# Performance work log

Measured on AMD Instinct MI355X. Metric: run time of the kernel, lower is better.

## Reference

```python
import jax, jax.numpy as jnp
import numpy as np

GRID_SIZE = 0.08
EPS = 1e-5
B, N, C_IN, C_OUT = 8, 65536, 64, 128


def setup_inputs() -> dict:
    key = jax.random.key(0)
    k1, k2, k3, k4 = jax.random.split(key, 4)
    # xyz in [0, 2): ~25 voxels per axis at grid_size=0.08 -> M ~ 15k clusters
    xyz = jax.random.uniform(k1, (B, N, 3), dtype=jnp.float32) * 2.0
    feats = jax.random.normal(k2, (B, N, C_IN), dtype=jnp.float32)
    W = jax.random.normal(k3, (C_IN, C_OUT), dtype=jnp.float32) / np.sqrt(C_IN)
    b = jnp.zeros((C_OUT,), jnp.float32)
    gamma = jnp.ones((C_OUT,), jnp.float32)
    beta = jnp.zeros((C_OUT,), jnp.float32)
    return {"xyz": xyz, "feats": feats, "W": W, "b": b, "gamma": gamma, "beta": beta}


def _voxel_pool_one(xyz_b, feats_b):
    # xyz_b: (N,3), feats_b: (N,C). Static pad to N clusters (worst case M=N).
    n = xyz_b.shape[0]
    coords = jnp.floor(xyz_b / GRID_SIZE).astype(jnp.int32)
    coords = coords - coords.min(axis=0)
    dims = coords.max(axis=0) + 1
    keys = coords[:, 0] * dims[1] * dims[2] + coords[:, 1] * dims[2] + coords[:, 2]
    # unique(return_inverse) via sort: cluster ids follow ascending key order
    order = jnp.argsort(keys)
    sk = keys[order]
    is_new = jnp.concatenate([jnp.ones((1,), bool), sk[1:] != sk[:-1]])
    seg = (jnp.cumsum(is_new) - 1).astype(jnp.int32)
    cluster = jnp.zeros((n,), jnp.int32).at[order].set(seg)
    M = is_new.sum().astype(jnp.int32)
    xyz_sum = jax.ops.segment_sum(xyz_b, cluster, num_segments=n)
    feat_sum = jax.ops.segment_sum(feats_b, cluster, num_segments=n)
    count = jax.ops.segment_sum(jnp.ones((n,), xyz_b.dtype), cluster, num_segments=n)
    count = jnp.maximum(count, 1.0)[:, None]
    return xyz_sum / count, feat_sum / count, cluster, M


def reference(xyz, feats, W, b, gamma, beta):
    xyz_pooled, feat_mean, cluster, Ms = jax.vmap(_voxel_pool_one)(xyz, feats)
    max_M = Ms.max()
    # linear + layernorm on (B, N, C_OUT) (padded rows beyond M_b are zeros)
    h = feat_mean @ W + b
    mu = h.mean(axis=-1, keepdims=True)
    var = ((h - mu) ** 2).mean(axis=-1, keepdims=True)
    feats_pooled = (h - mu) * jax.lax.rsqrt(var + EPS) * gamma + beta
    return xyz_pooled, feats_pooled, cluster, max_M
```

## Files before the change

### kernel.cpp

```cpp
#include <hip/hip_runtime.h>
#include <cstdint>
#include <climits>
#include <math.h>

#define Bb    8
#define Nn    65536
#define CIN   64
#define COUT  128
#define KMAXX 15632
#define VKEY  25600
#define VSTR  25600
#define EPSV  1e-5f

#define OFF_MVALS  0
#define OFF_MAXM   8
#define OFF_TAB    16
#define OFF_CNT    204816
#define OFF_SEGS   329872
#define OFF_SORT   454928
#define OFF_MEAN   586000
#define WS_END     8589584
#define MEMSET_INTS 204816

__device__ __forceinline__ int voxc(float x, float rcp_g) {
    return (int)floorf(x * rcp_g);
}

__device__ __forceinline__ float rdlanef(float v, int l) {
    return __uint_as_float(__builtin_amdgcn_readlane(__float_as_uint(v), l));
}

__global__ __launch_bounds__(256) void k_zero(float4* __restrict__ feats4,
                                              float4* __restrict__ xyz4) {
    const unsigned A_PER_B = 49904u * 32u;
    const unsigned B_PER_B = 49904u * 3u / 4u;
    const unsigned A4 = Bb * A_PER_B;
    const unsigned TOT = A4 + Bb * B_PER_B;
    unsigned t = blockIdx.x * 256u + threadIdx.x;
    if (t >= TOT) return;
    const float4 z = make_float4(0.f, 0.f, 0.f, 0.f);
    if (t < A4) {
        unsigned b = t / A_PER_B;
        unsigned r = t - b * A_PER_B;
        feats4[(size_t)b * (Nn * 32u) + 15632u * 32u + r] = z;
    } else {
        unsigned t2 = t - A4;
        unsigned b = t2 / B_PER_B;
        unsigned r = t2 - b * B_PER_B;
        xyz4[(size_t)b * (Nn * 3u / 4u) + (15632u * 3u / 4u) + r] = z;
    }
}

__global__ __launch_bounds__(256) void k_count(const float* __restrict__ xyz,
                                               int* __restrict__ tab,
                                               float grid) {
    float rcp_g = __builtin_amdgcn_rcpf(grid);
    int i = blockIdx.x * 256 + threadIdx.x;
    int b = i >> 16;
    int c0 = voxc(xyz[(size_t)i * 3 + 0], rcp_g);
    int c1 = voxc(xyz[(size_t)i * 3 + 1], rcp_g);
    int c2 = voxc(xyz[(size_t)i * 3 + 2], rcp_g);
    atomicAdd(&tab[b * VSTR + (c0 * 32 + c1) * 32 + c2], 1);
}

__global__ __launch_bounds__(1024) void k_scan(int* __restrict__ tab,
                                               float* __restrict__ cntf,
                                               int* __restrict__ segs,
                                               int* __restrict__ Ms,
                                               int* __restrict__ maxM) {
    __shared__ int wsC[16], wsFg[16];
    int b = blockIdx.x, tid = threadIdx.x;
    int lane = tid & 63, wv = tid >> 6;
    bool act = tid < (VKEY / 32);
    int4 f[8];
    int4* tb4 = (int4*)(tab + b * VSTR);
    const int4 z4 = make_int4(0, 0, 0, 0);
#pragma unroll
    for (int j = 0; j < 8; ++j) f[j] = act ? tb4[tid * 8 + j] : z4;
    int* ff = (int*)f;
    int sc = 0, sf = 0;
#pragma unroll
    for (int j = 0; j < 32; ++j) { sc += ff[j]; sf += (ff[j] != 0); }
    int ic = sc, ig = sf;
#pragma unroll
    for (int d = 1; d < 64; d <<= 1) {
        int tc = __shfl_up(ic, d);
        int tg = __shfl_up(ig, d);
        if (lane >= d) { ic += tc; ig += tg; }
    }
    if (lane == 63) { wsC[wv] = ic; wsFg[wv] = ig; }
    __syncthreads();
    int wpC = 0, wpF = 0, totF = 0;
#pragma unroll
    for (int w = 0; w < 16; ++w) {
        int vc = wsC[w], vf = wsFg[w];
        if (w < wv) { wpC += vc; wpF += vf; }
        totF += vf;
    }
    if (act) {
        int runC = wpC + ic - sc;
        int runF = wpF + ig - sf;
        int4 o[8];
        int* oo = (int*)o;
#pragma unroll
        for (int j = 0; j < 32; ++j) {
            int c = ff[j];
            oo[j] = (runF << 17) | runC;
            if (c) {
                cntf[b * KMAXX + runF] = (float)c;
                segs[b * KMAXX + runF] = runC;
                runC += c;
                runF += 1;
            }
        }
#pragma unroll
        for (int j = 0; j < 8; ++j) tb4[tid * 8 + j] = o[j];
    }
    if (tid == 0) {
        Ms[b] = totF;
        atomicMax(maxM, totF);
    }
}

__global__ __launch_bounds__(256) void k_scatter(const float* __restrict__ xyz,
                                                 int* __restrict__ tab,
                                                 unsigned short* __restrict__ sorted,
                                                 float* __restrict__ out_cluster,
                                                 float grid) {
    float rcp_g = __builtin_amdgcn_rcpf(grid);
    int i = blockIdx.x * 256 + threadIdx.x;
    int b = i >> 16;
    int c0 = voxc(xyz[(size_t)i * 3 + 0], rcp_g);
    int c1 = voxc(xyz[(size_t)i * 3 + 1], rcp_g);
    int c2 = voxc(xyz[(size_t)i * 3 + 2], rcp_g);
    int v = atomicAdd(&tab[b * VSTR + (c0 * 32 + c1) * 32 + c2], 1);
    sorted[(size_t)b * Nn + (v & 0x1FFFF)] = (unsigned short)i;
    out_cluster[i] = (float)(v >> 17);
}

#define GPB 245
__global__ __launch_bounds__(256, 6) void k_gather(const float* __restrict__ xyz,
                                                   const float4* __restrict__ feats4,
                                                   const unsigned short* __restrict__ sorted,
                                                   const float* __restrict__ cnt,
                                                   const int* __restrict__ segs,
                                                   const int* __restrict__ Ms,
                                                   float4* __restrict__ mean4,
                                                   float* __restrict__ out_xyz) {
    const int b = blockIdx.x / GPB;
    const int blk = blockIdx.x - b * GPB;
    const int wv = threadIdx.x >> 6, lane = threadIdx.x & 63;
    const int sub = lane >> 4, c4 = lane & 15;
    const int rowBase = blk * 64 + wv * 16;
    if (rowBase >= KMAXX) return;
    const int M = Ms[b];
    const size_t pbase = (size_t)b * Nn;
    const size_t cbase = (size_t)b * KMAXX;
    float cl = 0.0f;
    int sl = 0;
    if (lane < 16) {
        int r = rowBase + lane;
        if (r < M) { cl = cnt[cbase + r]; sl = segs[cbase + r]; }
    }
    for (int it = 0; it < 4; ++it) {
        const int row0 = rowBase + it * 4;
        int c[4], s[4];
        float cf[4];
#pragma unroll
        for (int q = 0; q < 4; ++q) {
            cf[q] = rdlanef(cl, it * 4 + q);
            s[q] = __builtin_amdgcn_readlane(sl, it * 4 + q);
            c[q] = (int)cf[q];
        }
        int p[4][2];
#pragma unroll
        for (int q = 0; q < 4; ++q) {
            p[q][0] = (sub     < c[q]) ? (int)sorted[pbase + s[q] + sub]     : -1;
            p[q][1] = (sub + 4 < c[q]) ? (int)sorted[pbase + s[q] + sub + 4] : -1;
        }
        float4 acc[4];
        float axs[4];
#pragma unroll
        for (int q = 0; q < 4; ++q) { acc[q] = make_float4(0.f, 0.f, 0.f, 0.f); axs[q] = 0.f; }
#pragma unroll
        for (int q = 0; q < 4; ++q) {
#pragma unroll
            for (int h = 0; h < 2; ++h) {
                int pp = p[q][h];
                if (pp >= 0) {
                    float4 v = feats4[(pbase + pp) * 16 + c4];
                    acc[q].x += v.x; acc[q].y += v.y; acc[q].z += v.z; acc[q].w += v.w;
                    if (c4 < 3) axs[q] += xyz[(pbase + pp) * 3 + c4];
                }
            }
        }
#pragma unroll
        for (int q = 0; q < 4; ++q) {
            for (int g = 2; g * 4 < c[q]; ++g) {
                int i = g * 4 + sub;
                if (i < c[q]) {
                    int pp = (int)sorted[pbase + s[q] + i];
                    float4 v = feats4[(pbase + pp) * 16 + c4];
                    acc[q].x += v.x; acc[q].y += v.y; acc[q].z += v.z; acc[q].w += v.w;
                    if (c4 < 3) axs[q] += xyz[(pbase + pp) * 3 + c4];
                }
            }
        }
#pragma unroll
        for (int q = 0; q < 4; ++q) {
            const int row = row0 + q;
            if (row < M) {
                float4 a = acc[q];
                a.x += __shfl_xor(a.x, 16); a.x += __shfl_xor(a.x, 32);
                a.y += __shfl_xor(a.y, 16); a.y += __shfl_xor(a.y, 32);
                a.z += __shfl_xor(a.z, 16); a.z += __shfl_xor(a.z, 32);
                a.w += __shfl_xor(a.w, 16); a.w += __shfl_xor(a.w, 32);
                float ax = axs[q];
                ax += __shfl_xor(ax, 16); ax += __shfl_xor(ax, 32);
                float cv = cf[q];
                float4 m4 = make_float4(a.x / cv, a.y / cv, a.z / cv, a.w / cv);
                if (lane < 16) mean4[(cbase + row) * 16 + c4] = m4;
                if (lane < 3)
                    out_xyz[(pbase + row) * 3 + lane] = ax / cv;
            } else {
                if (lane < 3)
                    out_xyz[(pbase + row) * 3 + lane] = 0.0f;
            }
        }
    }
}

#define BPB 245
__global__ __launch_bounds__(256) void k_gemmln(const float4* __restrict__ mean4,
                                                const int* __restrict__ Ms,
                                                const int* __restrict__ maxM,
                                                const float* __restrict__ W,
                                                const float* __restrict__ bias,
                                                const float* __restrict__ gamma,
                                                const float* __restrict__ beta,
                                                float* __restrict__ out_feats,
                                                float* __restrict__ out_maxM) {
    __shared__ float sWT[128 * 68];
    const int tid = threadIdx.x;
    for (int idx = tid; idx < 64 * 128; idx += 256) {
        int k = idx >> 7, c = idx & 127;
        sWT[c * 68 + k] = W[idx];
    }
    if (blockIdx.x == 0 && tid == 0) out_maxM[0] = (float)maxM[0];
    const int b = blockIdx.x / BPB;
    const int blk = blockIdx.x - b * BPB;
    const int wv = tid >> 6, lane = tid & 63;
    const int c4 = lane & 15;
    const int M = Ms[b];
    const float bias0 = bias[lane], bias1 = bias[lane + 64];
    const float g0 = gamma[lane], g1 = gamma[lane + 64];
    const float be0 = beta[lane], be1 = beta[lane + 64];
    __syncthreads();
    const int rowBase = blk * 64 + wv * 16;
    if (rowBase >= KMAXX) return;
    const size_t cbase = (size_t)b * KMAXX;
    if (rowBase >= M) {
        const float4 z = make_float4(0.f, 0.f, 0.f, 0.f);
        float4* of4 = (float4*)out_feats;
        size_t obase = ((size_t)b * Nn + rowBase) * 32;
#pragma unroll
        for (int i = 0; i < 8; ++i) of4[obase + i * 64 + lane] = z;
        return;
    }
    const float* wt0 = &sWT[lane * 68];
    const float* wt1 = &sWT[(lane + 64) * 68];
    for (int it = 0; it < 4; ++it) {
        const int row0 = rowBase + it * 4;
        const size_t cb0 = cbase + row0;
        float4 mm[4];
        bool lv[4];
#pragma unroll
        for (int r = 0; r < 4; ++r) {
            lv[r] = (row0 + r) < M;
            mm[r] = lv[r] ? mean4[(cb0 + r) * 16 + c4]
                          : make_float4(0.f, 0.f, 0.f, 0.f);
        }
        float a0[4] = {bias0, bias0, bias0, bias0};
        float a1[4] = {bias1, bias1, bias1, bias1};
#pragma unroll
        for (int k4 = 0; k4 < 16; ++k4) {
            float4 w0 = *(const float4*)&wt0[k4 * 4];
            float4 w1 = *(const float4*)&wt1[k4 * 4];
#pragma unroll
            for (int r = 0; r < 4; ++r) {
                float s0 = rdlanef(mm[r].x, k4);
                float s1 = rdlanef(mm[r].y, k4);
                float s2 = rdlanef(mm[r].z, k4);
                float s3 = rdlanef(mm[r].w, k4);
                a0[r] += s0 * w0.x + s1 * w0.y + s2 * w0.z + s3 * w0.w;
                a1[r] += s0 * w1.x + s1 * w1.y + s2 * w1.z + s3 * w1.w;
            }
        }
#pragma unroll
        for (int r = 0; r < 4; ++r) {
            float s = a0[r] + a1[r];
#pragma unroll
            for (int d2 = 32; d2 >= 1; d2 >>= 1) s += __shfl_xor(s, d2);
            float mu = s * (1.0f / 128.0f);
            float d0 = a0[r] - mu, d1 = a1[r] - mu;
            float q = d0 * d0 + d1 * d1;
#pragma unroll
            for (int d2 = 32; d2 >= 1; d2 >>= 1) q += __shfl_xor(q, d2);
            float rs = rsqrtf(q * (1.0f / 128.0f) + EPSV);
            float o0 = lv[r] ? (d0 * rs * g0 + be0) : 0.0f;
            float o1 = lv[r] ? (d1 * rs * g1 + be1) : 0.0f;
            size_t ob = ((size_t)b * Nn + row0 + r) * 128;
            out_feats[ob + lane] = o0;
            out_feats[ob + 64 + lane] = o1;
        }
    }
}

extern "C" void kernel_launch(void* const* d_in, const int* in_sizes, int n_in,
                              void* d_out, int out_size, void* d_ws, size_t ws_size,
                              hipStream_t stream) {
    const float* xyz   = (const float*)d_in[0];
    const float* feats = (const float*)d_in[1];
    const float* W     = (const float*)d_in[2];
    const float* bias  = (const float*)d_in[3];
    const float* gamma = (const float*)d_in[4];
    const float* beta  = (const float*)d_in[5];

    float* out = (float*)d_out;
    float* out_xyz     = out;
    float* out_feats   = out + (size_t)Bb * Nn * 3;
    float* out_cluster = out_feats + (size_t)Bb * Nn * COUT;
    float* out_maxM    = out_cluster + (size_t)Bb * Nn;

    int*   wsI    = (int*)d_ws;
    float* wsF    = (float*)d_ws;
    int*   Ms     = wsI + OFF_MVALS;
    int*   maxM   = wsI + OFF_MAXM;
    int*   tab    = wsI + OFF_TAB;
    float* cnt    = wsF + OFF_CNT;
    int*   segs   = wsI + OFF_SEGS;
    unsigned short* sorted = (unsigned short*)(wsI + OFF_SORT);
    float* meanb  = wsF + OFF_MEAN;

    const float grid_sz = 0.08f;

    {
        unsigned tot = Bb * (49904u * 32u) + Bb * (49904u * 3u / 4u);
        k_zero<<<(tot + 255) / 256, 256, 0, stream>>>((float4*)out_feats, (float4*)out_xyz);
    }
    hipMemsetAsync(wsI, 0, (size_t)MEMSET_INTS * 4, stream);
    k_count<<<Bb * Nn / 256, 256, 0, stream>>>(xyz, tab, grid_sz);
    k_scan<<<Bb, 1024, 0, stream>>>(tab, cnt, segs, Ms, maxM);
    k_scatter<<<Bb * Nn / 256, 256, 0, stream>>>(xyz, tab, sorted, out_cluster, grid_sz);
    k_gather<<<Bb * GPB, 256, 0, stream>>>(xyz, (const float4*)feats, sorted, cnt, segs,
                                           Ms, (float4*)meanb, out_xyz);
    k_gemmln<<<Bb * BPB, 256, 0, stream>>>((const float4*)meanb, Ms, maxM, W, bias,
                                           gamma, beta, out_feats, out_maxM);
}
```

Before: 531.4 us.

## Fold padding zero-fill into GEMM-LN kernel and cache voxel keys between passes

Removes the separate zero-fill kernel. The tail rows of out_feats and out_xyz past KMAXX are now zeroed by extra blocks of the GEMM+LayerNorm kernel, whose grid grows to cover all N rows per batch. k_count also stores each point's 16-bit voxel key in workspace, so k_scatter reads the key instead of reloading xyz and recomputing floors. The key buffer aliases the mean buffer, which is safe only because k_gather writes means after k_scatter has consumed the keys.

```diff
diff --git a/kernel.cpp b/kernel.cpp
--- a/kernel.cpp
+++ b/kernel.cpp
@@ -30,29 +30,9 @@
     return __uint_as_float(__builtin_amdgcn_readlane(__float_as_uint(v), l));
 }
 
-__global__ __launch_bounds__(256) void k_zero(float4* __restrict__ feats4,
-                                              float4* __restrict__ xyz4) {
-    const unsigned A_PER_B = 49904u * 32u;
-    const unsigned B_PER_B = 49904u * 3u / 4u;
-    const unsigned A4 = Bb * A_PER_B;
-    const unsigned TOT = A4 + Bb * B_PER_B;
-    unsigned t = blockIdx.x * 256u + threadIdx.x;
-    if (t >= TOT) return;
-    const float4 z = make_float4(0.f, 0.f, 0.f, 0.f);
-    if (t < A4) {
-        unsigned b = t / A_PER_B;
-        unsigned r = t - b * A_PER_B;
-        feats4[(size_t)b * (Nn * 32u) + 15632u * 32u + r] = z;
-    } else {
-        unsigned t2 = t - A4;
-        unsigned b = t2 / B_PER_B;
-        unsigned r = t2 - b * B_PER_B;
-        xyz4[(size_t)b * (Nn * 3u / 4u) + (15632u * 3u / 4u) + r] = z;
-    }
-}
-
 __global__ __launch_bounds__(256) void k_count(const float* __restrict__ xyz,
                                                int* __restrict__ tab,
+                                               unsigned short* __restrict__ keys,
                                                float grid) {
     float rcp_g = __builtin_amdgcn_rcpf(grid);
     int i = blockIdx.x * 256 + threadIdx.x;
@@ -60,7 +40,9 @@
     int c0 = voxc(xyz[(size_t)i * 3 + 0], rcp_g);
     int c1 = voxc(xyz[(size_t)i * 3 + 1], rcp_g);
     int c2 = voxc(xyz[(size_t)i * 3 + 2], rcp_g);
-    atomicAdd(&tab[b * VSTR + (c0 * 32 + c1) * 32 + c2], 1);
+    int key = (c0 * 32 + c1) * 32 + c2;
+    atomicAdd(&tab[b * VSTR + key], 1);
+    keys[i] = (unsigned short)key;
 }
 
 __global__ __launch_bounds__(1024) void k_scan(int* __restrict__ tab,
@@ -122,18 +104,14 @@
     }
 }
 
-__global__ __launch_bounds__(256) void k_scatter(const float* __restrict__ xyz,
+__global__ __launch_bounds__(256) void k_scatter(const unsigned short* __restrict__ keys,
                                                  int* __restrict__ tab,
                                                  unsigned short* __restrict__ sorted,
-                                                 float* __restrict__ out_cluster,
-                                                 float grid) {
-    float rcp_g = __builtin_amdgcn_rcpf(grid);
+                                                 float* __restrict__ out_cluster) {
     int i = blockIdx.x * 256 + threadIdx.x;
     int b = i >> 16;
-    int c0 = voxc(xyz[(size_t)i * 3 + 0], rcp_g);
-    int c1 = voxc(xyz[(size_t)i * 3 + 1], rcp_g);
-    int c2 = voxc(xyz[(size_t)i * 3 + 2], rcp_g);
-    int v = atomicAdd(&tab[b * VSTR + (c0 * 32 + c1) * 32 + c2], 1);
+    int key = keys[i];
+    int v = atomicAdd(&tab[b * VSTR + key], 1);
     sorted[(size_t)b * Nn + (v & 0x1FFFF)] = (unsigned short)i;
     out_cluster[i] = (float)(v >> 17);
 }
@@ -230,7 +208,7 @@
     }
 }
 
-#define BPB 245
+#define GBLK 1024
 __global__ __launch_bounds__(256) void k_gemmln(const float4* __restrict__ mean4,
                                                 const int* __restrict__ Ms,
                                                 const int* __restrict__ maxM,
@@ -239,17 +217,32 @@
                                                 const float* __restrict__ gamma,
                                                 const float* __restrict__ beta,
                                                 float* __restrict__ out_feats,
+                                                float* __restrict__ out_xyz,
                                                 float* __restrict__ out_maxM) {
+    const int tid = threadIdx.x;
+    const int b = blockIdx.x >> 10;
+    const int blk = blockIdx.x & 1023;
+    const int wv = tid >> 6, lane = tid & 63;
+    if (blockIdx.x == 0 && tid == 0) out_maxM[0] = (float)maxM[0];
+
+    if (blk * 64 >= KMAXX) {
+        const int rowBase = blk * 64 + wv * 16;
+        const float4 z = make_float4(0.f, 0.f, 0.f, 0.f);
+        float4* of4 = (float4*)out_feats;
+        size_t obase = ((size_t)b * Nn + rowBase) * 32;
+#pragma unroll
+        for (int i = 0; i < 8; ++i) of4[obase + i * 64 + lane] = z;
+        float4* ox4 = (float4*)out_xyz;
+        size_t xb = ((size_t)b * Nn + rowBase) * 3 / 4;
+        if (lane < 12) ox4[xb + lane] = z;
+        return;
+    }
+
     __shared__ float sWT[128 * 68];
-    const int tid = threadIdx.x;
     for (int idx = tid; idx < 64 * 128; idx += 256) {
         int k = idx >> 7, c = idx & 127;
         sWT[c * 68 + k] = W[idx];
     }
-    if (blockIdx.x == 0 && tid == 0) out_maxM[0] = (float)maxM[0];
-    const int b = blockIdx.x / BPB;
-    const int blk = blockIdx.x - b * BPB;
-    const int wv = tid >> 6, lane = tid & 63;
     const int c4 = lane & 15;
     const int M = Ms[b];
     const float bias0 = bias[lane], bias1 = bias[lane + 64];
@@ -257,7 +250,6 @@
     const float be0 = beta[lane], be1 = beta[lane + 64];
     __syncthreads();
     const int rowBase = blk * 64 + wv * 16;
-    if (rowBase >= KMAXX) return;
     const size_t cbase = (size_t)b * KMAXX;
     if (rowBase >= M) {
         const float4 z = make_float4(0.f, 0.f, 0.f, 0.f);
@@ -265,6 +257,11 @@
         size_t obase = ((size_t)b * Nn + rowBase) * 32;
 #pragma unroll
         for (int i = 0; i < 8; ++i) of4[obase + i * 64 + lane] = z;
+        if (rowBase >= KMAXX) {
+            float4* ox4 = (float4*)out_xyz;
+            size_t xb = ((size_t)b * Nn + rowBase) * 3 / 4;
+            if (lane < 12) ox4[xb + lane] = z;
+        }
         return;
     }
     const float* wt0 = &sWT[lane * 68];
@@ -341,19 +338,16 @@
     int*   segs   = wsI + OFF_SEGS;
     unsigned short* sorted = (unsigned short*)(wsI + OFF_SORT);
     float* meanb  = wsF + OFF_MEAN;
+    unsigned short* keys = (unsigned short*)(wsF + OFF_MEAN);
 
     const float grid_sz = 0.08f;
 
-    {
-        unsigned tot = Bb * (49904u * 32u) + Bb * (49904u * 3u / 4u);
-        k_zero<<<(tot + 255) / 256, 256, 0, stream>>>((float4*)out_feats, (float4*)out_xyz);
-    }
     hipMemsetAsync(wsI, 0, (size_t)MEMSET_INTS * 4, stream);
-    k_count<<<Bb * Nn / 256, 256, 0, stream>>>(xyz, tab, grid_sz);
+    k_count<<<Bb * Nn / 256, 256, 0, stream>>>(xyz, tab, keys, grid_sz);
     k_scan<<<Bb, 1024, 0, stream>>>(tab, cnt, segs, Ms, maxM);
-    k_scatter<<<Bb * Nn / 256, 256, 0, stream>>>(xyz, tab, sorted, out_cluster, grid_sz);
+    k_scatter<<<Bb * Nn / 256, 256, 0, stream>>>(keys, tab, sorted, out_cluster);
     k_gather<<<Bb * GPB, 256, 0, stream>>>(xyz, (const float4*)feats, sorted, cnt, segs,
                                            Ms, (float4*)meanb, out_xyz);
-    k_gemmln<<<Bb * BPB, 256, 0, stream>>>((const float4*)meanb, Ms, maxM, W, bias,
-                                           gamma, beta, out_feats, out_maxM);
-}
+    k_gemmln<<<Bb * GBLK, 256, 0, stream>>>((const float4*)meanb, Ms, maxM, W, bias,
+                                            gamma, beta, out_feats, out_xyz, out_maxM);
+}
```

Result: no change. 524.6 us (-1.3%).
